# Optimization experiments

Hardware: AMD Instinct MI355X
Metric: run time of the kernel (lower is better)

## Reference

```python
import jax, jax.numpy as jnp
import numpy as np

N_NODES = 50000
N_EDGES = 800000
F_DIM = 256
H_DIM = 256
O_DIM = 64


def spmm(edge_index, edge_weight, x):
    # sparse adj (COO) @ dense x: out[dst] += w * x[src]
    src = edge_index[0]
    dst = edge_index[1]
    msgs = edge_weight[:, None] * x[src]          # [E, D]
    return jax.ops.segment_sum(msgs, dst, num_segments=x.shape[0])


def setup_inputs() -> dict:
    key = jax.random.key(0)
    ks = jax.random.split(key, 10)
    stdv = 1.0 / np.sqrt(H_DIM)
    u = lambda k, shp: jax.random.uniform(k, shp, jnp.float32, -stdv, stdv)
    return {
        "input": jax.random.normal(ks[0], (N_NODES, F_DIM), jnp.float32),
        "edge_index": jax.random.randint(ks[1], (2, N_EDGES), 0, N_NODES, jnp.int32),
        "edge_weight": jax.random.uniform(ks[2], (N_EDGES,), jnp.float32),
        "mixture_weight": u(ks[3], (1,)),
        "hidden_weight": u(ks[4], (F_DIM, H_DIM)),
        "hidden_bias": u(ks[5], (H_DIM,)),
        "mean_weight": u(ks[6], (H_DIM, O_DIM)),
        "mean_bias": u(ks[7], (O_DIM,)),
        "log_std_weight": u(ks[8], (H_DIM, O_DIM)),
        "log_std_bias": u(ks[9], (O_DIM,)),
    }


def reference(input, edge_index, edge_weight, mixture_weight, hidden_weight,
              hidden_bias, mean_weight, mean_bias, log_std_weight, log_std_bias):
    # eval mode: dropout is identity
    # --- GCN branch ---
    support = input @ hidden_weight                       # [N, H]
    hidden_g = jax.nn.relu(spmm(edge_index, edge_weight, support) + hidden_bias)
    mean_gcn = spmm(edge_index, edge_weight, hidden_g @ mean_weight)      # [N, O]
    log_std_gcn = spmm(edge_index, edge_weight, hidden_g @ log_std_weight)
    # --- MLP branch ---
    hidden_m = jax.nn.relu(support + hidden_bias)
    mean_mlp = hidden_m @ mean_weight + mean_bias
    log_std_mlp = hidden_m @ log_std_weight + log_std_bias
    # --- mixture (note: z_mean uses raw weight, z_log_std uses sigmoid, as in source) ---
    mw = mixture_weight
    mr = jax.nn.sigmoid(mixture_weight)
    z_mean = mean_gcn * mw + mean_mlp * (1.0 - mw)
    z_log_std = log_std_gcn * mr + log_std_mlp * (1.0 - mr)
    return (z_mean, z_log_std)
```

## Files before the change

### kernel.cpp

```cpp
#include <hip/hip_runtime.h>
#include <math.h>

#define NN 50000
#define NE 800000
#define KD 256
#define OD 64
#define NCH ((NN + 255) / 256)
#define EPB 4096
#define NBLK ((NE + EPB - 1) / EPB)
#define NHT (NCH * NBLK)

#define QS 32.0f
#define IQS (1.0f / 32.0f)
#define QS2 16.0f
#define IQS2 (1.0f / 16.0f)

using bf16x8 = __attribute__((ext_vector_type(8))) short;
using f32x4  = __attribute__((ext_vector_type(4))) float;

__device__ __forceinline__ unsigned short f2b(float x) {
    union { float f; unsigned u; } c; c.f = x;
    unsigned r = (c.u + 0x7FFF + ((c.u >> 16) & 1)) >> 16;
    return (unsigned short)r;
}
__device__ __forceinline__ float b2f(unsigned short b) {
    union { unsigned u; float f; } c; c.u = ((unsigned)b) << 16;
    return c.f;
}
__device__ __forceinline__ signed char quant8(float v) {
    int q = __float2int_rn(v * QS);
    q = q > 127 ? 127 : (q < -127 ? -127 : q);
    return (signed char)q;
}
__device__ __forceinline__ unsigned quant16u(float v) {
    int q = __float2int_rn(v * QS2);
    return (unsigned)(q > 127 ? 127 : q);
}


__global__ __launch_bounds__(256) void k_hist(const int* __restrict__ dst,
                                              int* __restrict__ histT) {
    __shared__ int bins[NCH];
    int t = threadIdx.x, blk = blockIdx.x;
    if (t < NCH) bins[t] = 0;
    __syncthreads();
    int base = blk * EPB;
    #pragma unroll
    for (int i = 0; i < EPB / 256; ++i) {
        int e = base + i * 256 + t;
        if (e < NE) atomicAdd(&bins[dst[e] >> 8], 1);
    }
    __syncthreads();
    if (t < NCH) histT[t * NBLK + blk] = bins[t];
}

__global__ __launch_bounds__(256) void k_scanbins(int* __restrict__ histT,
                                                  int* __restrict__ binSum) {
    __shared__ int s[256];
    int bin = blockIdx.x, t = threadIdx.x;
    int v = (t < NBLK) ? histT[bin * NBLK + t] : 0;
    s[t] = v;
    __syncthreads();
    for (int o = 1; o < 256; o <<= 1) {
        int x = (t >= o) ? s[t - o] : 0;
        __syncthreads();
        s[t] += x;
        __syncthreads();
    }
    if (t < NBLK) histT[bin * NBLK + t] = s[t] - v;
    if (t == NBLK - 1) binSum[bin] = s[t];
}

__global__ void k_binscan(const int* __restrict__ binSum, int* __restrict__ binPrefix) {
    __shared__ int s[256];
    int t = threadIdx.x;
    int v = (t < NCH) ? binSum[t] : 0;
    s[t] = v;
    __syncthreads();
    for (int o = 1; o < 256; o <<= 1) {
        int x = (t >= o) ? s[t - o] : 0;
        __syncthreads();
        s[t] += x;
        __syncthreads();
    }
    if (t < NCH) binPrefix[t] = s[t] - v;
    if (t == NCH - 1) binPrefix[NCH] = s[t];
}

__global__ __launch_bounds__(256) void k_bucketw(const int* __restrict__ src,
                                                 const int* __restrict__ dst,
                                                 const float* __restrict__ w,
                                                 const int* __restrict__ histT,
                                                 const int* __restrict__ binPrefix,
                                                 int2* __restrict__ bkt) {
    __shared__ int cur[NCH];
    int t = threadIdx.x, blk = blockIdx.x;
    if (t < NCH) cur[t] = histT[t * NBLK + blk] + binPrefix[t];
    __syncthreads();
    int base = blk * EPB;
    #pragma unroll
    for (int i = 0; i < EPB / 256; ++i) {
        int e = base + i * 256 + t;
        if (e < NE) {
            int d = dst[e];
            int p = atomicAdd(&cur[d >> 8], 1);
            bkt[p] = make_int2((d << 16) | src[e], __float_as_int(w[e]));
        }
    }
}

__global__ __launch_bounds__(256) void k_deg2(const int2* __restrict__ bkt,
                                              const int* __restrict__ binPrefix,
                                              int* __restrict__ deg,
                                              int* __restrict__ chunkSum8) {
    __shared__ int cnt[256];
    __shared__ int s[256];
    int t = threadIdx.x, b = blockIdx.x;
    cnt[t] = 0;
    __syncthreads();
    int e0 = binPrefix[b], e1 = binPrefix[b + 1];
    for (int e = e0 + t; e < e1; e += 256)
        atomicAdd(&cnt[(((unsigned)bkt[e].x) >> 16) & 255], 1);
    __syncthreads();
    int node = b * 256 + t;
    int c = cnt[t];
    if (node < NN) deg[node] = c;
    s[t] = (node < NN) ? ((c + 7) & ~7) : 0;
    __syncthreads();
    for (int o = 128; o > 0; o >>= 1) {
        if (t < o) s[t] += s[t + o];
        __syncthreads();
    }
    if (t == 0) chunkSum8[b] = s[0];
}

__global__ void k_scan_chunks(const int* __restrict__ chunkSum8, int* __restrict__ chunkOff8) {
    __shared__ int s[256];
    int t = threadIdx.x;
    int v = (t < NCH) ? chunkSum8[t] : 0;
    s[t] = v;
    __syncthreads();
    for (int o = 1; o < 256; o <<= 1) {
        int x = (t >= o) ? s[t - o] : 0;
        __syncthreads();
        s[t] += x;
        __syncthreads();
    }
    if (t < NCH) chunkOff8[t] = s[t] - v;
    if (t == NCH - 1) chunkOff8[NCH] = s[t];
}

__global__ __launch_bounds__(256) void k_place2f(const int2* __restrict__ bkt,
                                                 const int* __restrict__ binPrefix,
                                                 const int* __restrict__ chunkOff8,
                                                 const int* __restrict__ deg,
                                                 int* __restrict__ offsets8,
                                                 int2* __restrict__ pedge) {
    __shared__ int s[256];
    __shared__ int ncur[256];
    int t = threadIdx.x, b = blockIdx.x;
    int node = b * 256 + t;
    int dv = (node < NN) ? deg[node] : 0;
    int pv = (dv + 7) & ~7;
    s[t] = pv;
    __syncthreads();
    for (int o = 1; o < 256; o <<= 1) {
        int x = (t >= o) ? s[t - o] : 0;
        __syncthreads();
        s[t] += x;
        __syncthreads();
    }
    int excl = s[t] - pv + chunkOff8[b];
    if (node <= NN) offsets8[node] = excl;
    ncur[t] = excl;
    __syncthreads();
    int e0 = binPrefix[b], e1 = binPrefix[b + 1];
    for (int e = e0 + t; e < e1; e += 256) {
        int2 v = bkt[e];
        int d = ((unsigned)v.x) >> 16;
        int p = atomicAdd(&ncur[d & 255], 1);
        pedge[p] = v;
    }
    __syncthreads();
    if (node < NN) {
        int p0 = ncur[t];
        int p1 = excl + pv;
        for (int p = p0; p < p1; ++p) pedge[p] = make_int2(0, 0);
    }
}


__global__ void k_convW(const float* __restrict__ hw, const float* __restrict__ mw_,
                        const float* __restrict__ lw,
                        unsigned short* __restrict__ Wht, unsigned short* __restrict__ Wmlt) {
    int idx = blockIdx.x * 256 + threadIdx.x;
    if (idx < 256 * 256) {
        int n = idx >> 8, k = idx & 255;
        Wht[(size_t)n * 256 + k] = f2b(hw[(size_t)k * 256 + n]);
    }
    if (idx < 128 * 256) {
        int n = idx >> 8, k = idx & 255;
        float v = (n < 64) ? mw_[(size_t)k * 64 + n] : lw[(size_t)k * 64 + (n - 64)];
        Wmlt[(size_t)n * 256 + k] = f2b(v);
    }
}


template <int AM, int EM>
__global__ __launch_bounds__(256) void k_gemm(const void* __restrict__ Ap,
                                              const unsigned short* __restrict__ Bt,
                                              const float* __restrict__ hbias,
                                              const float* __restrict__ mbias,
                                              const float* __restrict__ lbias,
                                              void* __restrict__ Outp,
                                              void* __restrict__ Outp2) {
    __shared__ unsigned short As[64 * 64];
    __shared__ unsigned short Bs[128 * 64];
    const int tid = threadIdx.x;
    const int row0 = blockIdx.x * 64;
    const int n0 = blockIdx.y * 128;
    const int lane = tid & 63;
    const int w = tid >> 6, wm = w >> 1, wn = w & 1;
    const int lr = lane & 15, lg = lane >> 4;
    const int rA = tid >> 2;
    const int qA = tid & 3;
    const int rB = tid >> 1;
    const int hB = tid & 1;

    f32x4 acc[2][4] = {};

    for (int k0 = 0; k0 < KD; k0 += 64) {
        {
            int gr = row0 + rA;
            unsigned short tmp[16];
            if (AM == 0) {
                const float* A = (const float*)Ap;
                if (gr < NN) {
                    #pragma unroll
                    for (int i = 0; i < 4; ++i) {
                        float4 v = *reinterpret_cast<const float4*>(
                            &A[(size_t)gr * KD + k0 + qA * 16 + i * 4]);
                        tmp[i * 4 + 0] = f2b(v.x); tmp[i * 4 + 1] = f2b(v.y);
                        tmp[i * 4 + 2] = f2b(v.z); tmp[i * 4 + 3] = f2b(v.w);
                    }
                } else {
                    #pragma unroll
                    for (int i = 0; i < 16; ++i) tmp[i] = 0;
                }
            } else if (AM == 2) {
                const unsigned short* A = (const unsigned short*)Ap;
                if (gr < NN) {
                    *reinterpret_cast<uint4*>(&tmp[0]) =
                        *reinterpret_cast<const uint4*>(&A[(size_t)gr * KD + k0 + qA * 16]);
                    *reinterpret_cast<uint4*>(&tmp[8]) =
                        *reinterpret_cast<const uint4*>(&A[(size_t)gr * KD + k0 + qA * 16 + 8]);
                    #pragma unroll
                    for (int i = 0; i < 4; ++i) {
                        float4 hb4 = *reinterpret_cast<const float4*>(&hbias[k0 + qA * 16 + i * 4]);
                        tmp[i * 4 + 0] = f2b(fmaxf(b2f(tmp[i * 4 + 0]) + hb4.x, 0.f));
                        tmp[i * 4 + 1] = f2b(fmaxf(b2f(tmp[i * 4 + 1]) + hb4.y, 0.f));
                        tmp[i * 4 + 2] = f2b(fmaxf(b2f(tmp[i * 4 + 2]) + hb4.z, 0.f));
                        tmp[i * 4 + 3] = f2b(fmaxf(b2f(tmp[i * 4 + 3]) + hb4.w, 0.f));
                    }
                } else {
                    #pragma unroll
                    for (int i = 0; i < 16; ++i) tmp[i] = 0;
                }
            } else {
                const signed char* A = (const signed char*)Ap;
                if (gr < NN) {
                    signed char q[16];
                    *reinterpret_cast<uint4*>(q) =
                        *reinterpret_cast<const uint4*>(&A[(size_t)gr * KD + k0 + qA * 16]);
                    #pragma unroll
                    for (int i = 0; i < 16; ++i) tmp[i] = f2b((float)q[i] * IQS2);
                } else {
                    #pragma unroll
                    for (int i = 0; i < 16; ++i) tmp[i] = 0;
                }
            }
            int s0 = (qA * 2) ^ (rA & 7);
            int s1 = (qA * 2 + 1) ^ (rA & 7);
            *reinterpret_cast<uint4*>(&As[rA * 64 + s0 * 8]) = *reinterpret_cast<const uint4*>(&tmp[0]);
            *reinterpret_cast<uint4*>(&As[rA * 64 + s1 * 8]) = *reinterpret_cast<const uint4*>(&tmp[8]);
        }
        {
            const unsigned short* B = Bt + (size_t)(n0 + rB) * KD + k0 + hB * 32;
            #pragma unroll
            for (int i = 0; i < 4; ++i) {
                uint4 u = *reinterpret_cast<const uint4*>(B + i * 8);
                int slot = (hB * 4 + i) ^ (rB & 7);
                *reinterpret_cast<uint4*>(&Bs[rB * 64 + slot * 8]) = u;
            }
        }
        __syncthreads();
        #pragma unroll
        for (int ks = 0; ks < 2; ++ks) {
            int slot = ks * 4 + lg;
            bf16x8 a[2], b[4];
            #pragma unroll
            for (int fm = 0; fm < 2; ++fm) {
                int ra = wm * 32 + fm * 16 + lr;
                a[fm] = *reinterpret_cast<const bf16x8*>(&As[ra * 64 + ((slot ^ (ra & 7))) * 8]);
            }
            #pragma unroll
            for (int fn = 0; fn < 4; ++fn) {
                int rb = wn * 64 + fn * 16 + lr;
                b[fn] = *reinterpret_cast<const bf16x8*>(&Bs[rb * 64 + ((slot ^ (rb & 7))) * 8]);
            }
            #pragma unroll
            for (int fm = 0; fm < 2; ++fm)
                #pragma unroll
                for (int fn = 0; fn < 4; ++fn)
                    acc[fm][fn] = __builtin_amdgcn_mfma_f32_16x16x32_bf16(a[fm], b[fn], acc[fm][fn], 0, 0, 0);
        }
        __syncthreads();
    }
    #pragma unroll
    for (int fm = 0; fm < 2; ++fm) {
        #pragma unroll
        for (int j = 0; j < 4; ++j) {
            int grow = row0 + wm * 32 + fm * 16 + lg * 4 + j;
            if (grow >= NN) continue;
            #pragma unroll
            for (int fn = 0; fn < 4; ++fn) {
                int gcol = n0 + wn * 64 + fn * 16 + lr;
                float v = acc[fm][fn][j];
                if (EM == 2) {
                    ((unsigned short*)Outp)[(size_t)grow * 256 + gcol] = f2b(v);
                    ((signed char*)Outp2)[(size_t)grow * 256 + gcol] = quant8(v);
                } else if (EM == 3) {
                    ((signed char*)Outp)[(size_t)grow * 128 + gcol] = quant8(v);
                } else {
                    float b = (gcol < 64) ? mbias[gcol] : lbias[gcol - 64];
                    ((unsigned short*)Outp)[(size_t)grow * 128 + gcol] = f2b(v + b);
                }
            }
        }
    }
}


__global__ __launch_bounds__(256) void k_spmm1(const int* __restrict__ off8,
                                               const int2* __restrict__ pedge,
                                               const unsigned* __restrict__ supq,
                                               const float* __restrict__ bias,
                                               unsigned* __restrict__ hgq) {
    int lane = threadIdx.x & 63;
    int wid = blockIdx.x * 4 + (threadIdx.x >> 6);
    int d0 = wid * 2, d1 = d0 + 1;
    int ea = off8[d0], eA = off8[d0 + 1], eB = off8[d0 + 2];
    int eb = eA;
    float a0 = 0.f, a1 = 0.f, a2 = 0.f, a3 = 0.f;
    float c0 = 0.f, c1 = 0.f, c2 = 0.f, c3 = 0.f;
    for (; ea < eA && eb < eB; ea += 8, eb += 8) {
        int2 Ea[8], Eb[8];
        unsigned Ua[8], Ub[8];
        #pragma unroll
        for (int i = 0; i < 8; ++i) { Ea[i] = pedge[ea + i]; Eb[i] = pedge[eb + i]; }
        #pragma unroll
        for (int i = 0; i < 8; ++i) {
            Ua[i] = supq[(size_t)(Ea[i].x & 0xffff) * 64 + lane];
            Ub[i] = supq[(size_t)(Eb[i].x & 0xffff) * 64 + lane];
        }
        #pragma unroll
        for (int i = 0; i < 8; ++i) {
            float wa = __int_as_float(Ea[i].y), wb = __int_as_float(Eb[i].y);
            unsigned ua = Ua[i], ub = Ub[i];
            a0 = fmaf(wa, (float)((int)(signed char)(ua)), a0);
            a1 = fmaf(wa, (float)((int)(signed char)(ua >> 8)), a1);
            a2 = fmaf(wa, (float)((int)(signed char)(ua >> 16)), a2);
            a3 = fmaf(wa, (float)((int)(signed char)(ua >> 24)), a3);
            c0 = fmaf(wb, (float)((int)(signed char)(ub)), c0);
            c1 = fmaf(wb, (float)((int)(signed char)(ub >> 8)), c1);
            c2 = fmaf(wb, (float)((int)(signed char)(ub >> 16)), c2);
            c3 = fmaf(wb, (float)((int)(signed char)(ub >> 24)), c3);
        }
    }
    for (; ea < eA; ea += 8) {
        int2 E[8]; unsigned U[8];
        #pragma unroll
        for (int i = 0; i < 8; ++i) E[i] = pedge[ea + i];
        #pragma unroll
        for (int i = 0; i < 8; ++i) U[i] = supq[(size_t)(E[i].x & 0xffff) * 64 + lane];
        #pragma unroll
        for (int i = 0; i < 8; ++i) {
            float w = __int_as_float(E[i].y); unsigned u = U[i];
            a0 = fmaf(w, (float)((int)(signed char)(u)), a0);
            a1 = fmaf(w, (float)((int)(signed char)(u >> 8)), a1);
            a2 = fmaf(w, (float)((int)(signed char)(u >> 16)), a2);
            a3 = fmaf(w, (float)((int)(signed char)(u >> 24)), a3);
        }
    }
    for (; eb < eB; eb += 8) {
        int2 E[8]; unsigned U[8];
        #pragma unroll
        for (int i = 0; i < 8; ++i) E[i] = pedge[eb + i];
        #pragma unroll
        for (int i = 0; i < 8; ++i) U[i] = supq[(size_t)(E[i].x & 0xffff) * 64 + lane];
        #pragma unroll
        for (int i = 0; i < 8; ++i) {
            float w = __int_as_float(E[i].y); unsigned u = U[i];
            c0 = fmaf(w, (float)((int)(signed char)(u)), c0);
            c1 = fmaf(w, (float)((int)(signed char)(u >> 8)), c1);
            c2 = fmaf(w, (float)((int)(signed char)(u >> 16)), c2);
            c3 = fmaf(w, (float)((int)(signed char)(u >> 24)), c3);
        }
    }
    float4 b = *reinterpret_cast<const float4*>(&bias[lane * 4]);
    unsigned oa = quant16u(fmaxf(a0 * IQS + b.x, 0.f))
                | (quant16u(fmaxf(a1 * IQS + b.y, 0.f)) << 8)
                | (quant16u(fmaxf(a2 * IQS + b.z, 0.f)) << 16)
                | (quant16u(fmaxf(a3 * IQS + b.w, 0.f)) << 24);
    unsigned oc = quant16u(fmaxf(c0 * IQS + b.x, 0.f))
                | (quant16u(fmaxf(c1 * IQS + b.y, 0.f)) << 8)
                | (quant16u(fmaxf(c2 * IQS + b.z, 0.f)) << 16)
                | (quant16u(fmaxf(c3 * IQS + b.w, 0.f)) << 24);
    hgq[(size_t)d0 * 64 + lane] = oa;
    hgq[(size_t)d1 * 64 + lane] = oc;
}


__global__ __launch_bounds__(256) void k_spmm2(const int* __restrict__ off8,
                                               const int2* __restrict__ pedge,
                                               const unsigned short* __restrict__ gq,
                                               const unsigned short* __restrict__ mlp,
                                               const float* __restrict__ mixw,
                                               float* __restrict__ out) {
    int lane = threadIdx.x & 63;
    int wid = blockIdx.x * 4 + (threadIdx.x >> 6);
    int d0 = wid * 2, d1 = d0 + 1;
    int ea = off8[d0], eA = off8[d0 + 1], eB = off8[d0 + 2];
    int eb = eA;
    float a0 = 0.f, a1 = 0.f, c0 = 0.f, c1 = 0.f;
    for (; ea < eA && eb < eB; ea += 8, eb += 8) {
        int2 Ea[8], Eb[8];
        unsigned short Ua[8], Ub[8];
        #pragma unroll
        for (int i = 0; i < 8; ++i) { Ea[i] = pedge[ea + i]; Eb[i] = pedge[eb + i]; }
        #pragma unroll
        for (int i = 0; i < 8; ++i) {
            Ua[i] = gq[(size_t)(Ea[i].x & 0xffff) * 64 + lane];
            Ub[i] = gq[(size_t)(Eb[i].x & 0xffff) * 64 + lane];
        }
        #pragma unroll
        for (int i = 0; i < 8; ++i) {
            float wa = __int_as_float(Ea[i].y), wb = __int_as_float(Eb[i].y);
            a0 = fmaf(wa, (float)((int)(signed char)(Ua[i] & 0xff)), a0);
            a1 = fmaf(wa, (float)((int)(signed char)(Ua[i] >> 8)), a1);
            c0 = fmaf(wb, (float)((int)(signed char)(Ub[i] & 0xff)), c0);
            c1 = fmaf(wb, (float)((int)(signed char)(Ub[i] >> 8)), c1);
        }
    }
    for (; ea < eA; ea += 8) {
        int2 E[8]; unsigned short U[8];
        #pragma unroll
        for (int i = 0; i < 8; ++i) E[i] = pedge[ea + i];
        #pragma unroll
        for (int i = 0; i < 8; ++i) U[i] = gq[(size_t)(E[i].x & 0xffff) * 64 + lane];
        #pragma unroll
        for (int i = 0; i < 8; ++i) {
            float w = __int_as_float(E[i].y);
            a0 = fmaf(w, (float)((int)(signed char)(U[i] & 0xff)), a0);
            a1 = fmaf(w, (float)((int)(signed char)(U[i] >> 8)), a1);
        }
    }
    for (; eb < eB; eb += 8) {
        int2 E[8]; unsigned short U[8];
        #pragma unroll
        for (int i = 0; i < 8; ++i) E[i] = pedge[eb + i];
        #pragma unroll
        for (int i = 0; i < 8; ++i) U[i] = gq[(size_t)(E[i].x & 0xffff) * 64 + lane];
        #pragma unroll
        for (int i = 0; i < 8; ++i) {
            float w = __int_as_float(E[i].y);
            c0 = fmaf(w, (float)((int)(signed char)(U[i] & 0xff)), c0);
            c1 = fmaf(w, (float)((int)(signed char)(U[i] >> 8)), c1);
        }
    }
    float mw = mixw[0];
    float mr = 1.f / (1.f + expf(-mw));
    int c = lane * 2;
    ushort2 mu0 = reinterpret_cast<const ushort2*>(mlp)[(size_t)d0 * 64 + lane];
    ushort2 mu1 = reinterpret_cast<const ushort2*>(mlp)[(size_t)d1 * 64 + lane];
    float g00 = a0 * IQS, g01 = a1 * IQS;
    float g10 = c0 * IQS, g11 = c1 * IQS;
    if (c < 64) {
        *reinterpret_cast<float2*>(out + (size_t)d0 * OD + c) =
            make_float2(g00 * mw + b2f(mu0.x) * (1.f - mw), g01 * mw + b2f(mu0.y) * (1.f - mw));
        *reinterpret_cast<float2*>(out + (size_t)d1 * OD + c) =
            make_float2(g10 * mw + b2f(mu1.x) * (1.f - mw), g11 * mw + b2f(mu1.y) * (1.f - mw));
    } else {
        float* ol = out + (size_t)NN * OD;
        *reinterpret_cast<float2*>(ol + (size_t)d0 * OD + (c - 64)) =
            make_float2(g00 * mr + b2f(mu0.x) * (1.f - mr), g01 * mr + b2f(mu0.y) * (1.f - mr));
        *reinterpret_cast<float2*>(ol + (size_t)d1 * OD + (c - 64)) =
            make_float2(g10 * mr + b2f(mu1.x) * (1.f - mr), g11 * mr + b2f(mu1.y) * (1.f - mr));
    }
}


extern "C" void kernel_launch(void* const* d_in, const int* in_sizes, int n_in,
                              void* d_out, int out_size, void* d_ws, size_t ws_size,
                              hipStream_t stream) {
    const float* input = (const float*)d_in[0];
    const int*   ei    = (const int*)d_in[1];
    const float* ew    = (const float*)d_in[2];
    const float* mixw  = (const float*)d_in[3];
    const float* hw    = (const float*)d_in[4];
    const float* hb    = (const float*)d_in[5];
    const float* mw_   = (const float*)d_in[6];
    const float* mb    = (const float*)d_in[7];
    const float* lw    = (const float*)d_in[8];
    const float* lb    = (const float*)d_in[9];
    float* out = (float*)d_out;

    const int* src = ei;
    const int* dst = ei + NE;

    char* ws = (char*)d_ws;
    size_t off = 0;
    auto alloc = [&](size_t bytes) -> void* {
        void* p = ws + off;
        off += (bytes + 255) & ~(size_t)255;
        return p;
    };
    int*   deg      = (int*)alloc((size_t)NN * 4);
    int*   offsets8 = (int*)alloc((size_t)(NN + 2) * 4);
    int*   chunkSum8= (int*)alloc((size_t)NCH * 4);
    int*   chunkOff8= (int*)alloc((size_t)(NCH + 1) * 4);
    int*   binSum   = (int*)alloc((size_t)NCH * 4);
    int*   binPrefix= (int*)alloc((size_t)(NCH + 1) * 4);
    int*   histT    = (int*)alloc((size_t)NHT * 4);
    int2*  bkt      = (int2*)alloc((size_t)NE * 8);
    int2*  pedge    = (int2*)alloc(((size_t)NE + 8 * NN) * 8);
    unsigned short* Wht  = (unsigned short*)alloc((size_t)256 * 256 * 2);
    unsigned short* Wmlt = (unsigned short*)alloc((size_t)128 * 256 * 2);
    unsigned short* support  = (unsigned short*)alloc((size_t)NN * KD * 2);
    signed char*    supq     = (signed char*)alloc((size_t)NN * KD);
    signed char*    hgq      = (signed char*)alloc((size_t)NN * KD);
    signed char*    gcnq     = (signed char*)alloc((size_t)NN * 128);
    unsigned short* mlp      = (unsigned short*)alloc((size_t)NN * 128 * 2);

    k_hist<<<NBLK, 256, 0, stream>>>(dst, histT);
    k_scanbins<<<NCH, 256, 0, stream>>>(histT, binSum);
    k_binscan<<<1, 256, 0, stream>>>(binSum, binPrefix);
    k_bucketw<<<NBLK, 256, 0, stream>>>(src, dst, ew, histT, binPrefix, bkt);
    k_deg2<<<NCH, 256, 0, stream>>>(bkt, binPrefix, deg, chunkSum8);
    k_scan_chunks<<<1, 256, 0, stream>>>(chunkSum8, chunkOff8);
    k_place2f<<<NCH, 256, 0, stream>>>(bkt, binPrefix, chunkOff8, deg, offsets8, pedge);

    k_convW<<<256, 256, 0, stream>>>(hw, mw_, lw, Wht, Wmlt);

    int mblk = (NN + 63) / 64;
    k_gemm<0, 2><<<dim3(mblk, 2), 256, 0, stream>>>(input, Wht, hb, mb, lb, support, supq);
    k_spmm1<<<NN / 8, 256, 0, stream>>>(offsets8, pedge, (const unsigned*)supq, hb, (unsigned*)hgq);
    k_gemm<4, 3><<<dim3(mblk, 1), 256, 0, stream>>>(hgq, Wmlt, hb, mb, lb, gcnq, nullptr);
    k_gemm<2, 4><<<dim3(mblk, 1), 256, 0, stream>>>(support, Wmlt, hb, mb, lb, mlp, nullptr);
    k_spmm2<<<NN / 8, 256, 0, stream>>>(offsets8, pedge, (const unsigned short*)gcnq, mlp, mixw, out);
}
```

Baseline: 158.4 us.

## Cut kernel launches by fusing scans, weight conversion and the two small GEMMs

Removes the single-block scan kernels. Each consumer block now recomputes the small prefix scans over bin and chunk sums in shared memory. Weight conversion is folded into the histogram launch as extra blocks, and the GCN and MLP projection GEMMs are merged into one launch selected by blockIdx.y. This cuts launch count and serialization gaps, at the cost of redundant per-block scans and extra barriers.

```diff
diff --git a/kernel.cpp b/kernel.cpp
--- a/kernel.cpp
+++ b/kernel.cpp
@@ -37,21 +37,49 @@
     return (unsigned)(q > 127 ? 127 : q);
 }
 
-
-__global__ __launch_bounds__(256) void k_hist(const int* __restrict__ dst,
-                                              int* __restrict__ histT) {
+__device__ __forceinline__ void blk_scan(int* s, int t) {
+    for (int o = 1; o < 256; o <<= 1) {
+        int x = (t >= o) ? s[t - o] : 0;
+        __syncthreads();
+        s[t] += x;
+        __syncthreads();
+    }
+}
+
+
+__global__ __launch_bounds__(256) void k_histconv(const int* __restrict__ dst,
+                                                  int* __restrict__ histT,
+                                                  const float* __restrict__ hw,
+                                                  const float* __restrict__ mw_,
+                                                  const float* __restrict__ lw,
+                                                  unsigned short* __restrict__ Wht,
+                                                  unsigned short* __restrict__ Wmlt) {
     __shared__ int bins[NCH];
-    int t = threadIdx.x, blk = blockIdx.x;
-    if (t < NCH) bins[t] = 0;
-    __syncthreads();
-    int base = blk * EPB;
-    #pragma unroll
-    for (int i = 0; i < EPB / 256; ++i) {
-        int e = base + i * 256 + t;
-        if (e < NE) atomicAdd(&bins[dst[e] >> 8], 1);
-    }
-    __syncthreads();
-    if (t < NCH) histT[t * NBLK + blk] = bins[t];
+    int t = threadIdx.x;
+    if (blockIdx.x < NBLK) {
+        int blk = blockIdx.x;
+        if (t < NCH) bins[t] = 0;
+        __syncthreads();
+        int base = blk * EPB;
+        #pragma unroll
+        for (int i = 0; i < EPB / 256; ++i) {
+            int e = base + i * 256 + t;
+            if (e < NE) atomicAdd(&bins[dst[e] >> 8], 1);
+        }
+        __syncthreads();
+        if (t < NCH) histT[t * NBLK + blk] = bins[t];
+    } else {
+        int idx = (blockIdx.x - NBLK) * 256 + t;
+        if (idx < 256 * 256) {
+            int n = idx >> 8, k = idx & 255;
+            Wht[(size_t)n * 256 + k] = f2b(hw[(size_t)k * 256 + n]);
+        }
+        if (idx < 128 * 256) {
+            int n = idx >> 8, k = idx & 255;
+            float v = (n < 64) ? mw_[(size_t)k * 64 + n] : lw[(size_t)k * 64 + (n - 64)];
+            Wmlt[(size_t)n * 256 + k] = f2b(v);
+        }
+    }
 }
 
 __global__ __launch_bounds__(256) void k_scanbins(int* __restrict__ histT,
@@ -61,41 +89,25 @@
     int v = (t < NBLK) ? histT[bin * NBLK + t] : 0;
     s[t] = v;
     __syncthreads();
-    for (int o = 1; o < 256; o <<= 1) {
-        int x = (t >= o) ? s[t - o] : 0;
-        __syncthreads();
-        s[t] += x;
-        __syncthreads();
-    }
+    blk_scan(s, t);
     if (t < NBLK) histT[bin * NBLK + t] = s[t] - v;
     if (t == NBLK - 1) binSum[bin] = s[t];
-}
-
-__global__ void k_binscan(const int* __restrict__ binSum, int* __restrict__ binPrefix) {
-    __shared__ int s[256];
-    int t = threadIdx.x;
-    int v = (t < NCH) ? binSum[t] : 0;
-    s[t] = v;
-    __syncthreads();
-    for (int o = 1; o < 256; o <<= 1) {
-        int x = (t >= o) ? s[t - o] : 0;
-        __syncthreads();
-        s[t] += x;
-        __syncthreads();
-    }
-    if (t < NCH) binPrefix[t] = s[t] - v;
-    if (t == NCH - 1) binPrefix[NCH] = s[t];
 }
 
 __global__ __launch_bounds__(256) void k_bucketw(const int* __restrict__ src,
                                                  const int* __restrict__ dst,
                                                  const float* __restrict__ w,
                                                  const int* __restrict__ histT,
-                                                 const int* __restrict__ binPrefix,
+                                                 const int* __restrict__ binSum,
                                                  int2* __restrict__ bkt) {
+    __shared__ int pre[256];
     __shared__ int cur[NCH];
     int t = threadIdx.x, blk = blockIdx.x;
-    if (t < NCH) cur[t] = histT[t * NBLK + blk] + binPrefix[t];
+    int v = (t < NCH) ? binSum[t] : 0;
+    pre[t] = v;
+    __syncthreads();
+    blk_scan(pre, t);
+    if (t < NCH) cur[t] = histT[t * NBLK + blk] + (pre[t] - v);
     __syncthreads();
     int base = blk * EPB;
     #pragma unroll
@@ -110,21 +122,26 @@
 }
 
 __global__ __launch_bounds__(256) void k_deg2(const int2* __restrict__ bkt,
-                                              const int* __restrict__ binPrefix,
+                                              const int* __restrict__ binSum,
                                               int* __restrict__ deg,
                                               int* __restrict__ chunkSum8) {
+    __shared__ int incl[256];
     __shared__ int cnt[256];
-    __shared__ int s[256];
     int t = threadIdx.x, b = blockIdx.x;
+    incl[t] = (t < NCH) ? binSum[t] : 0;
     cnt[t] = 0;
     __syncthreads();
-    int e0 = binPrefix[b], e1 = binPrefix[b + 1];
+    blk_scan(incl, t);
+    int e0 = (b > 0) ? incl[b - 1] : 0;
+    int e1 = incl[b];
+    __syncthreads();
     for (int e = e0 + t; e < e1; e += 256)
         atomicAdd(&cnt[(((unsigned)bkt[e].x) >> 16) & 255], 1);
     __syncthreads();
     int node = b * 256 + t;
     int c = cnt[t];
     if (node < NN) deg[node] = c;
+    __shared__ int s[256];
     s[t] = (node < NN) ? ((c + 7) & ~7) : 0;
     __syncthreads();
     for (int o = 128; o > 0; o >>= 1) {
@@ -134,47 +151,37 @@
     if (t == 0) chunkSum8[b] = s[0];
 }
 
-__global__ void k_scan_chunks(const int* __restrict__ chunkSum8, int* __restrict__ chunkOff8) {
-    __shared__ int s[256];
-    int t = threadIdx.x;
-    int v = (t < NCH) ? chunkSum8[t] : 0;
-    s[t] = v;
-    __syncthreads();
-    for (int o = 1; o < 256; o <<= 1) {
-        int x = (t >= o) ? s[t - o] : 0;
-        __syncthreads();
-        s[t] += x;
-        __syncthreads();
-    }
-    if (t < NCH) chunkOff8[t] = s[t] - v;
-    if (t == NCH - 1) chunkOff8[NCH] = s[t];
-}
-
 __global__ __launch_bounds__(256) void k_place2f(const int2* __restrict__ bkt,
-                                                 const int* __restrict__ binPrefix,
-                                                 const int* __restrict__ chunkOff8,
+                                                 const int* __restrict__ binSum,
+                                                 const int* __restrict__ chunkSum8,
                                                  const int* __restrict__ deg,
                                                  int* __restrict__ offsets8,
                                                  int2* __restrict__ pedge) {
+    __shared__ int binc[256];
+    __shared__ int cinc[256];
     __shared__ int s[256];
     __shared__ int ncur[256];
     int t = threadIdx.x, b = blockIdx.x;
+    binc[t] = (t < NCH) ? binSum[t] : 0;
+    __syncthreads();
+    blk_scan(binc, t);
+    cinc[t] = (t < NCH) ? chunkSum8[t] : 0;
+    __syncthreads();
+    blk_scan(cinc, t);
+    int e0 = (b > 0) ? binc[b - 1] : 0;
+    int e1 = binc[b];
+    int chunkBase = (b > 0) ? cinc[b - 1] : 0;
+    __syncthreads();
     int node = b * 256 + t;
     int dv = (node < NN) ? deg[node] : 0;
     int pv = (dv + 7) & ~7;
     s[t] = pv;
     __syncthreads();
-    for (int o = 1; o < 256; o <<= 1) {
-        int x = (t >= o) ? s[t - o] : 0;
-        __syncthreads();
-        s[t] += x;
-        __syncthreads();
-    }
-    int excl = s[t] - pv + chunkOff8[b];
+    blk_scan(s, t);
+    int excl = s[t] - pv + chunkBase;
     if (node <= NN) offsets8[node] = excl;
     ncur[t] = excl;
     __syncthreads();
-    int e0 = binPrefix[b], e1 = binPrefix[b + 1];
     for (int e = e0 + t; e < e1; e += 256) {
         int2 v = bkt[e];
         int d = ((unsigned)v.x) >> 16;
@@ -190,30 +197,10 @@
 }
 
 
-__global__ void k_convW(const float* __restrict__ hw, const float* __restrict__ mw_,
-                        const float* __restrict__ lw,
-                        unsigned short* __restrict__ Wht, unsigned short* __restrict__ Wmlt) {
-    int idx = blockIdx.x * 256 + threadIdx.x;
-    if (idx < 256 * 256) {
-        int n = idx >> 8, k = idx & 255;
-        Wht[(size_t)n * 256 + k] = f2b(hw[(size_t)k * 256 + n]);
-    }
-    if (idx < 128 * 256) {
-        int n = idx >> 8, k = idx & 255;
-        float v = (n < 64) ? mw_[(size_t)k * 64 + n] : lw[(size_t)k * 64 + (n - 64)];
-        Wmlt[(size_t)n * 256 + k] = f2b(v);
-    }
-}
-
-
-template <int AM, int EM>
-__global__ __launch_bounds__(256) void k_gemm(const void* __restrict__ Ap,
-                                              const unsigned short* __restrict__ Bt,
-                                              const float* __restrict__ hbias,
-                                              const float* __restrict__ mbias,
-                                              const float* __restrict__ lbias,
-                                              void* __restrict__ Outp,
-                                              void* __restrict__ Outp2) {
+__global__ __launch_bounds__(256) void k_gemm1(const float* __restrict__ Ap,
+                                               const unsigned short* __restrict__ Bt,
+                                               unsigned short* __restrict__ supOut,
+                                               signed char* __restrict__ supqOut) {
     __shared__ unsigned short As[64 * 64];
     __shared__ unsigned short Bs[128 * 64];
     const int tid = threadIdx.x;
@@ -222,10 +209,8 @@
     const int lane = tid & 63;
     const int w = tid >> 6, wm = w >> 1, wn = w & 1;
     const int lr = lane & 15, lg = lane >> 4;
-    const int rA = tid >> 2;
-    const int qA = tid & 3;
-    const int rB = tid >> 1;
-    const int hB = tid & 1;
+    const int rA = tid >> 2, qA = tid & 3;
+    const int rB = tid >> 1, hB = tid & 1;
 
     f32x4 acc[2][4] = {};
 
@@ -233,27 +218,104 @@
         {
             int gr = row0 + rA;
             unsigned short tmp[16];
-            if (AM == 0) {
-                const float* A = (const float*)Ap;
-                if (gr < NN) {
-                    #pragma unroll
-                    for (int i = 0; i < 4; ++i) {
-                        float4 v = *reinterpret_cast<const float4*>(
-                            &A[(size_t)gr * KD + k0 + qA * 16 + i * 4]);
-                        tmp[i * 4 + 0] = f2b(v.x); tmp[i * 4 + 1] = f2b(v.y);
-                        tmp[i * 4 + 2] = f2b(v.z); tmp[i * 4 + 3] = f2b(v.w);
-                    }
-                } else {
-                    #pragma unroll
-                    for (int i = 0; i < 16; ++i) tmp[i] = 0;
+            if (gr < NN) {
+                #pragma unroll
+                for (int i = 0; i < 4; ++i) {
+                    float4 v = *reinterpret_cast<const float4*>(
+                        &Ap[(size_t)gr * KD + k0 + qA * 16 + i * 4]);
+                    tmp[i * 4 + 0] = f2b(v.x); tmp[i * 4 + 1] = f2b(v.y);
+                    tmp[i * 4 + 2] = f2b(v.z); tmp[i * 4 + 3] = f2b(v.w);
                 }
-            } else if (AM == 2) {
-                const unsigned short* A = (const unsigned short*)Ap;
-                if (gr < NN) {
+            } else {
+                #pragma unroll
+                for (int i = 0; i < 16; ++i) tmp[i] = 0;
+            }
+            int s0 = (qA * 2) ^ (rA & 7);
+            int s1 = (qA * 2 + 1) ^ (rA & 7);
+            *reinterpret_cast<uint4*>(&As[rA * 64 + s0 * 8]) = *reinterpret_cast<const uint4*>(&tmp[0]);
+            *reinterpret_cast<uint4*>(&As[rA * 64 + s1 * 8]) = *reinterpret_cast<const uint4*>(&tmp[8]);
+        }
+        {
+            const unsigned short* B = Bt + (size_t)(n0 + rB) * KD + k0 + hB * 32;
+            #pragma unroll
+            for (int i = 0; i < 4; ++i) {
+                uint4 u = *reinterpret_cast<const uint4*>(B + i * 8);
+                int slot = (hB * 4 + i) ^ (rB & 7);
+                *reinterpret_cast<uint4*>(&Bs[rB * 64 + slot * 8]) = u;
+            }
+        }
+        __syncthreads();
+        #pragma unroll
+        for (int ks = 0; ks < 2; ++ks) {
+            int slot = ks * 4 + lg;
+            bf16x8 a[2], b[4];
+            #pragma unroll
+            for (int fm = 0; fm < 2; ++fm) {
+                int ra = wm * 32 + fm * 16 + lr;
+                a[fm] = *reinterpret_cast<const bf16x8*>(&As[ra * 64 + ((slot ^ (ra & 7))) * 8]);
+            }
+            #pragma unroll
+            for (int fn = 0; fn < 4; ++fn) {
+                int rb = wn * 64 + fn * 16 + lr;
+                b[fn] = *reinterpret_cast<const bf16x8*>(&Bs[rb * 64 + ((slot ^ (rb & 7))) * 8]);
+            }
+            #pragma unroll
+            for (int fm = 0; fm < 2; ++fm)
+                #pragma unroll
+                for (int fn = 0; fn < 4; ++fn)
+                    acc[fm][fn] = __builtin_amdgcn_mfma_f32_16x16x32_bf16(a[fm], b[fn], acc[fm][fn], 0, 0, 0);
+        }
+        __syncthreads();
+    }
+    #pragma unroll
+    for (int fm = 0; fm < 2; ++fm) {
+        #pragma unroll
+        for (int j = 0; j < 4; ++j) {
+            int grow = row0 + wm * 32 + fm * 16 + lg * 4 + j;
+            if (grow >= NN) continue;
+            #pragma unroll
+            for (int fn = 0; fn < 4; ++fn) {
+                int gcol = n0 + wn * 64 + fn * 16 + lr;
+                float v = acc[fm][fn][j];
+                supOut[(size_t)grow * 256 + gcol] = f2b(v);
+                supqOut[(size_t)grow * 256 + gcol] = quant8(v);
+            }
+        }
+    }
+}
+
+
+__global__ __launch_bounds__(256) void k_gemm2(const signed char* __restrict__ hgq,
+                                               const unsigned short* __restrict__ support,
+                                               const unsigned short* __restrict__ Bt,
+                                               const float* __restrict__ hbias,
+                                               const float* __restrict__ mbias,
+                                               const float* __restrict__ lbias,
+                                               signed char* __restrict__ gcnq,
+                                               unsigned short* __restrict__ mlpout) {
+    __shared__ unsigned short As[64 * 64];
+    __shared__ unsigned short Bs[128 * 64];
+    const bool mlpMode = blockIdx.y != 0;
+    const int tid = threadIdx.x;
+    const int row0 = blockIdx.x * 64;
+    const int lane = tid & 63;
+    const int w = tid >> 6, wm = w >> 1, wn = w & 1;
+    const int lr = lane & 15, lg = lane >> 4;
+    const int rA = tid >> 2, qA = tid & 3;
+    const int rB = tid >> 1, hB = tid & 1;
+
+    f32x4 acc[2][4] = {};
+
+    for (int k0 = 0; k0 < KD; k0 += 64) {
+        {
+            int gr = row0 + rA;
+            unsigned short tmp[16];
+            if (gr < NN) {
+                if (mlpMode) {
                     *reinterpret_cast<uint4*>(&tmp[0]) =
-                        *reinterpret_cast<const uint4*>(&A[(size_t)gr * KD + k0 + qA * 16]);
+                        *reinterpret_cast<const uint4*>(&support[(size_t)gr * KD + k0 + qA * 16]);
                     *reinterpret_cast<uint4*>(&tmp[8]) =
-                        *reinterpret_cast<const uint4*>(&A[(size_t)gr * KD + k0 + qA * 16 + 8]);
+                        *reinterpret_cast<const uint4*>(&support[(size_t)gr * KD + k0 + qA * 16 + 8]);
                     #pragma unroll
                     for (int i = 0; i < 4; ++i) {
                         float4 hb4 = *reinterpret_cast<const float4*>(&hbias[k0 + qA * 16 + i * 4]);
@@ -263,21 +325,15 @@
                         tmp[i * 4 + 3] = f2b(fmaxf(b2f(tmp[i * 4 + 3]) + hb4.w, 0.f));
                     }
                 } else {
+                    signed char q[16];
+                    *reinterpret_cast<uint4*>(q) =
+                        *reinterpret_cast<const uint4*>(&hgq[(size_t)gr * KD + k0 + qA * 16]);
                     #pragma unroll
-                    for (int i = 0; i < 16; ++i) tmp[i] = 0;
+                    for (int i = 0; i < 16; ++i) tmp[i] = f2b((float)q[i] * IQS2);
                 }
             } else {
-                const signed char* A = (const signed char*)Ap;
-                if (gr < NN) {
-                    signed char q[16];
-                    *reinterpret_cast<uint4*>(q) =
-                        *reinterpret_cast<const uint4*>(&A[(size_t)gr * KD + k0 + qA * 16]);
-                    #pragma unroll
-                    for (int i = 0; i < 16; ++i) tmp[i] = f2b((float)q[i] * IQS2);
-                } else {
-                    #pragma unroll
-                    for (int i = 0; i < 16; ++i) tmp[i] = 0;
-                }
+                #pragma unroll
+                for (int i = 0; i < 16; ++i) tmp[i] = 0;
             }
             int s0 = (qA * 2) ^ (rA & 7);
             int s1 = (qA * 2 + 1) ^ (rA & 7);
@@ -285,7 +341,7 @@
             *reinterpret_cast<uint4*>(&As[rA * 64 + s1 * 8]) = *reinterpret_cast<const uint4*>(&tmp[8]);
         }
         {
-            const unsigned short* B = Bt + (size_t)(n0 + rB) * KD + k0 + hB * 32;
+            const unsigned short* B = Bt + (size_t)rB * KD + k0 + hB * 32;
             #pragma unroll
             for (int i = 0; i < 4; ++i) {
                 uint4 u = *reinterpret_cast<const uint4*>(B + i * 8);
@@ -324,16 +380,13 @@
             if (grow >= NN) continue;
             #pragma unroll
             for (int fn = 0; fn < 4; ++fn) {
-                int gcol = n0 + wn * 64 + fn * 16 + lr;
+                int gcol = wn * 64 + fn * 16 + lr;
                 float v = acc[fm][fn][j];
-                if (EM == 2) {
-                    ((unsigned short*)Outp)[(size_t)grow * 256 + gcol] = f2b(v);
-                    ((signed char*)Outp2)[(size_t)grow * 256 + gcol] = quant8(v);
-                } else if (EM == 3) {
-                    ((signed char*)Outp)[(size_t)grow * 128 + gcol] = quant8(v);
+                if (mlpMode) {
+                    float b = (gcol < 64) ? mbias[gcol] : lbias[gcol - 64];
+                    mlpout[(size_t)grow * 128 + gcol] = f2b(v + b);
                 } else {
-                    float b = (gcol < 64) ? mbias[gcol] : lbias[gcol - 64];
-                    ((unsigned short*)Outp)[(size_t)grow * 128 + gcol] = f2b(v + b);
+                    gcnq[(size_t)grow * 128 + gcol] = quant8(v);
                 }
             }
         }
@@ -528,9 +581,7 @@
     int*   deg      = (int*)alloc((size_t)NN * 4);
     int*   offsets8 = (int*)alloc((size_t)(NN + 2) * 4);
     int*   chunkSum8= (int*)alloc((size_t)NCH * 4);
-    int*   chunkOff8= (int*)alloc((size_t)(NCH + 1) * 4);
     int*   binSum   = (int*)alloc((size_t)NCH * 4);
-    int*   binPrefix= (int*)alloc((size_t)(NCH + 1) * 4);
     int*   histT    = (int*)alloc((size_t)NHT * 4);
     int2*  bkt      = (int2*)alloc((size_t)NE * 8);
     int2*  pedge    = (int2*)alloc(((size_t)NE + 8 * NN) * 8);
@@ -542,20 +593,15 @@
     signed char*    gcnq     = (signed char*)alloc((size_t)NN * 128);
     unsigned short* mlp      = (unsigned short*)alloc((size_t)NN * 128 * 2);
 
-    k_hist<<<NBLK, 256, 0, stream>>>(dst, histT);
+    k_histconv<<<NBLK + 256, 256, 0, stream>>>(dst, histT, hw, mw_, lw, Wht, Wmlt);
     k_scanbins<<<NCH, 256, 0, stream>>>(histT, binSum);
-    k_binscan<<<1, 256, 0, stream>>>(binSum, binPrefix);
-    k_bucketw<<<NBLK, 256, 0, stream>>>(src, dst, ew, histT, binPrefix, bkt);
-    k_deg2<<<NCH, 256, 0, stream>>>(bkt, binPrefix, deg, chunkSum8);
-    k_scan_chunks<<<1, 256, 0, stream>>>(chunkSum8, chunkOff8);
-    k_place2f<<<NCH, 256, 0, stream>>>(bkt, binPrefix, chunkOff8, deg, offsets8, pedge);
-
-    k_convW<<<256, 256, 0, stream>>>(hw, mw_, lw, Wht, Wmlt);
+    k_bucketw<<<NBLK, 256, 0, stream>>>(src, dst, ew, histT, binSum, bkt);
+    k_deg2<<<NCH, 256, 0, stream>>>(bkt, binSum, deg, chunkSum8);
+    k_place2f<<<NCH, 256, 0, stream>>>(bkt, binSum, chunkSum8, deg, offsets8, pedge);
 
     int mblk = (NN + 63) / 64;
-    k_gemm<0, 2><<<dim3(mblk, 2), 256, 0, stream>>>(input, Wht, hb, mb, lb, support, supq);
+    k_gemm1<<<dim3(mblk, 2), 256, 0, stream>>>(input, Wht, support, supq);
     k_spmm1<<<NN / 8, 256, 0, stream>>>(offsets8, pedge, (const unsigned*)supq, hb, (unsigned*)hgq);
-    k_gemm<4, 3><<<dim3(mblk, 1), 256, 0, stream>>>(hgq, Wmlt, hb, mb, lb, gcnq, nullptr);
-    k_gemm<2, 4><<<dim3(mblk, 1), 256, 0, stream>>>(support, Wmlt, hb, mb, lb, mlp, nullptr);
+    k_gemm2<<<dim3(mblk, 2), 256, 0, stream>>>(hgq, support, Wmlt, hb, mb, lb, gcnq, mlp);
     k_spmm2<<<NN / 8, 256, 0, stream>>>(offsets8, pedge, (const unsigned short*)gcnq, mlp, mixw, out);
 }
```

Result: no change. 155.7 us (-1.7%).
